# Performance work log

Measured on AMD Instinct MI355X. Metric: run time of the kernel, lower is better.

## Reference

```python
import jax, jax.numpy as jnp
import numpy as np

EPS_NORM = 1e-6
EPS_Q = 1e-5


def rmsnorm(x, g):
    var = jnp.mean(jnp.square(x), axis=-1, keepdims=True)
    return x * jax.lax.rsqrt(var + EPS_NORM) * g


def act_quant(x):
    # per-token int8 absmax fake-quant (BitNet)
    scale = 127.0 / jnp.clip(jnp.max(jnp.abs(x), axis=-1, keepdims=True), EPS_Q, None)
    return jnp.clip(jnp.round(x * scale), -128.0, 127.0) / scale


def weight_quant(w):
    # per-tensor ternary (b1.58) fake-quant
    scale = 1.0 / jnp.clip(jnp.mean(jnp.abs(w)), EPS_Q, None)
    return jnp.clip(jnp.round(w * scale), -1.0, 1.0) / scale


def ste(x, fn):
    return x + jax.lax.stop_gradient(fn(x) - x)


def bitlinear(x, w, g):
    # RMSNorm -> act fake-quant (STE) -> ternary weight fake-quant (STE) -> matmul
    xn = rmsnorm(x, g)
    xq = ste(xn, act_quant)
    wq = ste(w, weight_quant)
    return jnp.einsum('bsd,od->bso', xq, wq)


def setup_inputs() -> dict:
    key = jax.random.key(0)
    k1, k2, k3 = jax.random.split(key, 3)
    B, S, D, I = 4, 4096, 2048, 5632
    x = jax.random.normal(k1, (B, S, D), dtype=jnp.float32)
    w_gate = jax.random.normal(k2, (2 * I, D), dtype=jnp.float32) * (D ** -0.5)
    g_gate = jnp.ones((D,), dtype=jnp.float32)
    w_down = jax.random.normal(k3, (D, I), dtype=jnp.float32) * (I ** -0.5)
    g_down = jnp.ones((I,), dtype=jnp.float32)
    return {"x": x, "w_gate": w_gate, "g_gate": g_gate,
            "w_down": w_down, "g_down": g_down}


def reference(x, w_gate, g_gate, w_down, g_down):
    y = bitlinear(x, w_gate, g_gate)            # [B, S, 2*I]
    gate, v = jnp.split(y, 2, axis=-1)          # chunk(2, -1)
    swiglu_out = gate * jax.nn.sigmoid(gate) * v  # swish(gate) * v
    z = bitlinear(swiglu_out, w_down, g_down)   # [B, S, D]
    return z
```

## Files before the change

### kernel.cpp

```cpp
#include <hip/hip_runtime.h>
#include <hip/hip_bf16.h>

typedef int v4i __attribute__((ext_vector_type(4)));

#define DEV __device__ __forceinline__

DEV void gload16(const void* g, void* l){
  __builtin_amdgcn_global_load_lds((const __attribute__((address_space(1))) unsigned int*)g,
                                   (__attribute__((address_space(3))) unsigned int*)l, 16, 0, 0);
}

DEV float block_sum256(float v, float* red){
#pragma unroll
  for (int o=32;o>0;o>>=1) v += __shfl_down(v,o);
  int w = threadIdx.x>>6;
  if ((threadIdx.x&63)==0) red[w]=v;
  __syncthreads();
  v = red[0]+red[1]+red[2]+red[3];
  __syncthreads();
  return v;
}
DEV float block_max256(float v, float* red){
#pragma unroll
  for (int o=32;o>0;o>>=1) v = fmaxf(v,__shfl_down(v,o));
  int w = threadIdx.x>>6;
  if ((threadIdx.x&63)==0) red[w]=v;
  __syncthreads();
  v = fmaxf(fmaxf(red[0],red[1]),fmaxf(red[2],red[3]));
  __syncthreads();
  return v;
}

__global__ __launch_bounds__(256) void reduce_abs_kernel(const float* __restrict__ w, long n4,
                                                         float* __restrict__ partials){
  __shared__ float red[4];
  const float4* w4 = (const float4*)w;
  float s = 0.f;
  for (long i = (long)blockIdx.x*256 + threadIdx.x; i < n4; i += (long)gridDim.x*256){
    float4 v = w4[i];
    s += fabsf(v.x)+fabsf(v.y)+fabsf(v.z)+fabsf(v.w);
  }
  s = block_sum256(s, red);
  if (threadIdx.x==0) partials[blockIdx.x]=s;
}

__global__ __launch_bounds__(256) void finalize_scales_kernel(const float* __restrict__ partials,
                                                              float* __restrict__ hdr){
  __shared__ float red[4];
  float s1=0.f, s2=0.f;
  for (int i=threadIdx.x;i<1024;i+=256){ s1+=partials[i]; s2+=partials[i+1024]; }
  s1 = block_sum256(s1, red);
  s2 = block_sum256(s2, red);
  if (threadIdx.x==0){
    float m1 = s1 / 23068672.0f;
    float sc1 = 1.0f / fmaxf(m1, 1e-5f);
    hdr[0]=sc1; hdr[1]=1.0f/sc1;
    float m2 = s2 / 11534336.0f;
    float sc2 = 1.0f / fmaxf(m2, 1e-5f);
    hdr[2]=sc2; hdr[3]=1.0f/sc2;
  }
}

__global__ __launch_bounds__(256) void quant_w_kernel(const float* __restrict__ w,
                                                      signed char* __restrict__ wq, long n4,
                                                      const float* __restrict__ hdr, int hi){
  float scale = hdr[hi];
  const float4* w4 = (const float4*)w;
  unsigned* o4 = (unsigned*)wq;
  for (long i = (long)blockIdx.x*256 + threadIdx.x; i < n4; i += (long)gridDim.x*256){
    float4 v = w4[i];
    int q0 = (int)fminf(fmaxf(rintf(v.x*scale),-1.f),1.f);
    int q1 = (int)fminf(fmaxf(rintf(v.y*scale),-1.f),1.f);
    int q2 = (int)fminf(fmaxf(rintf(v.z*scale),-1.f),1.f);
    int q3 = (int)fminf(fmaxf(rintf(v.w*scale),-1.f),1.f);
    unsigned pk = (q0&0xff) | ((q1&0xff)<<8) | ((q2&0xff)<<16) | ((q3&0xff)<<24);
    o4[i] = pk;
  }
}

__global__ __launch_bounds__(256) void rms_quant_x_kernel(const float* __restrict__ x,
                                                          const float* __restrict__ g,
                                                          signed char* __restrict__ xq,
                                                          float* __restrict__ isx){
  __shared__ float red[4];
  const int row = blockIdx.x, t = threadIdx.x;
  const float* xr = x + (size_t)row*2048 + t*8;
  float4 a = *(const float4*)xr;
  float4 b = *(const float4*)(xr+4);
  float xv[8] = {a.x,a.y,a.z,a.w,b.x,b.y,b.z,b.w};
  float ss = 0.f;
#pragma unroll
  for (int i=0;i<8;i++) ss += xv[i]*xv[i];
  ss = block_sum256(ss, red);
  float rs = rsqrtf(ss*(1.0f/2048.0f) + 1e-6f);
  const float* gr = g + t*8;
  float4 ga = *(const float4*)gr;
  float4 gb = *(const float4*)(gr+4);
  float gv[8] = {ga.x,ga.y,ga.z,ga.w,gb.x,gb.y,gb.z,gb.w};
  float xn[8]; float m = 0.f;
#pragma unroll
  for (int i=0;i<8;i++){ xn[i] = xv[i]*rs*gv[i]; m = fmaxf(m, fabsf(xn[i])); }
  m = block_max256(m, red);
  float scale = 127.0f / fmaxf(m, 1e-5f);
  unsigned long long pk = 0;
#pragma unroll
  for (int i=0;i<8;i++){
    int q = (int)fminf(fmaxf(rintf(xn[i]*scale), -128.0f), 127.0f);
    pk |= (unsigned long long)(unsigned char)(signed char)q << (8*i);
  }
  *(unsigned long long*)(xq + (size_t)row*2048 + t*8) = pk;
  if (t==0) isx[row] = 1.0f/scale;
}

__global__ __launch_bounds__(256) void rms_quant_sg_kernel(const __hip_bfloat16* __restrict__ sg,
                                                           const float* __restrict__ g,
                                                           signed char* __restrict__ xq,
                                                           float* __restrict__ isx){
  __shared__ float red[4];
  const int row = blockIdx.x, t = threadIdx.x;
  const unsigned* sr = (const unsigned*)(sg + (size_t)row*5632);
  float s[22];
  float ss = 0.f;
#pragma unroll
  for (int i=0;i<11;i++){
    unsigned u = sr[t + i*256];
    float f0 = __uint_as_float(u<<16);
    float f1 = __uint_as_float(u & 0xffff0000u);
    s[2*i]=f0; s[2*i+1]=f1;
    ss += f0*f0 + f1*f1;
  }
  ss = block_sum256(ss, red);
  float rs = rsqrtf(ss*(1.0f/5632.0f) + 1e-6f);
  const float2* g2 = (const float2*)g;
  float xn[22]; float m = 0.f;
#pragma unroll
  for (int i=0;i<11;i++){
    float2 gv = g2[t + i*256];
    xn[2*i]   = s[2*i]  *rs*gv.x;
    xn[2*i+1] = s[2*i+1]*rs*gv.y;
    m = fmaxf(m, fmaxf(fabsf(xn[2*i]), fabsf(xn[2*i+1])));
  }
  m = block_max256(m, red);
  float scale = 127.0f / fmaxf(m, 1e-5f);
  short* o2 = (short*)(xq + (size_t)row*5632);
#pragma unroll
  for (int i=0;i<11;i++){
    int q0 = (int)fminf(fmaxf(rintf(xn[2*i]  *scale), -128.0f), 127.0f);
    int q1 = (int)fminf(fmaxf(rintf(xn[2*i+1]*scale), -128.0f), 127.0f);
    o2[t + i*256] = (short)((q0 & 0xff) | ((q1 & 0xff) << 8));
  }
  if (t==0) isx[row] = 1.0f/scale;
}

__global__ __launch_bounds__(512) void gemm1_swiglu_kernel(const signed char* __restrict__ A,
                                                           const signed char* __restrict__ B,
                                                           const float* __restrict__ inv_sx,
                                                           const float* __restrict__ hdr,
                                                           __hip_bfloat16* __restrict__ out){
  constexpr int K = 2048;
  constexpr int NI = 5632;
  constexpr int NT = 32;
  __shared__ __align__(16) unsigned char smem[131072];

  const int t = threadIdx.x;
  const int lid = blockIdx.x + blockIdx.y * gridDim.x;
  const int xc = lid & 7;
  const int sx = lid >> 3;
  const int ch = sx >> 5;
  const int ii = sx & 31;
  const int bm0 = (xc*8 + (ii>>2)) * 256;
  const int bc0 = (ch*4 + (ii&3)) * 128;
  const int w = t >> 6, l = t & 63;
  const int ts = w >> 2;
  const int wv = w & 3;
  const int wr = wv * 64;
  const int lr = l & 15, lg = l >> 4;

  const float inv_sw = hdr[1];

  const signed char* aSrc[2]; int aOff[2];
#pragma unroll
  for (int i=0;i<2;i++){
    int c = t + i*512, r = c>>2, kp = c&3;
    aSrc[i] = A + (size_t)(bm0 + r)*K + ((kp ^ ((r>>1)&3))*16);
    aOff[i] = c*16;
  }
  const signed char* bSrc[2]; int bOff[2];
#pragma unroll
  for (int i=0;i<2;i++){
    int c = t + i*512, r = c>>2, kp = c&3;
    int grow = ((r>>7) ? NI : 0) + bc0 + (r&127);
    bSrc[i] = B + (size_t)grow*K + ((kp ^ ((r>>1)&3))*16);
    bOff[i] = 16384 + c*16;
  }
  int aoff[4];
#pragma unroll
  for (int i=0;i<4;i++){ int row = wr + i*16 + lr; aoff[i] = row*64 + ((lg ^ ((row>>1)&3))*16); }
  int boff[8];
#pragma unroll
  for (int j=0;j<8;j++){ int row = ts*128 + j*16 + lr; boff[j] = 16384 + row*64 + ((lg ^ ((row>>1)&3))*16); }

  v4i acc[4][8] = {};

#define STAGE1(BUF, KT) { unsigned char* _b = smem + (BUF)*32768;      \
    gload16(aSrc[0] + (KT)*64, _b + aOff[0]);                          \
    gload16(aSrc[1] + (KT)*64, _b + aOff[1]);                          \
    gload16(bSrc[0] + (KT)*64, _b + bOff[0]);                          \
    gload16(bSrc[1] + (KT)*64, _b + bOff[1]); }

#define COMP1(BUF) {                                                   \
  const signed char* _bs = (const signed char*)smem + (BUF)*32768;     \
  v4i af[4], bf[8];                                                    \
  _Pragma("unroll") for (int _i=0;_i<4;_i++) af[_i] = *(const v4i*)(_bs + aoff[_i]); \
  _Pragma("unroll") for (int _j=0;_j<8;_j++) bf[_j] = *(const v4i*)(_bs + boff[_j]); \
  __builtin_amdgcn_s_setprio(1);                                       \
  _Pragma("unroll") for (int _j=0;_j<8;_j++)                           \
    _Pragma("unroll") for (int _i=0;_i<4;_i++)                         \
      acc[_i][_j] = __builtin_amdgcn_mfma_i32_16x16x64_i8(af[_i], bf[_j], acc[_i][_j], 0, 0, 0); \
  __builtin_amdgcn_s_setprio(0);                                       \
}

  STAGE1(0,0); STAGE1(1,1); STAGE1(2,2);

  for (int kt = 0; kt < NT-2; ++kt){
    asm volatile("s_waitcnt vmcnt(8)" ::: "memory");
    __builtin_amdgcn_s_barrier();
    __builtin_amdgcn_sched_barrier(0);
    COMP1(kt&3);
    __builtin_amdgcn_sched_barrier(0);
    if (kt <= NT-4) STAGE1((kt+3)&3, kt+3);
  }
  asm volatile("s_waitcnt vmcnt(4)" ::: "memory");
  __builtin_amdgcn_s_barrier();
  __builtin_amdgcn_sched_barrier(0);
  COMP1((NT-2)&3);
  __builtin_amdgcn_sched_barrier(0);
  asm volatile("s_waitcnt vmcnt(0)" ::: "memory");
  __builtin_amdgcn_s_barrier();
  __builtin_amdgcn_sched_barrier(0);
  COMP1((NT-1)&3);
  __builtin_amdgcn_sched_barrier(0);

  float* vex = (float*)smem;
  __syncthreads();
  if (ts == 1){
#pragma unroll
    for (int i=0;i<4;i++){
#pragma unroll
      for (int r=0;r<4;r++){
        int lrow = wr + i*16 + lg*4 + r;
        float f = inv_sx[bm0 + lrow] * inv_sw;
#pragma unroll
        for (int j=0;j<8;j++)
          vex[lrow*128 + j*16 + lr] = (float)acc[i][j][r] * f;
      }
    }
  }
  __syncthreads();
  if (ts == 0){
#pragma unroll
    for (int i=0;i<4;i++){
#pragma unroll
      for (int r=0;r<4;r++){
        int lrow = wr + i*16 + lg*4 + r;
        float f = inv_sx[bm0 + lrow] * inv_sw;
#pragma unroll
        for (int j=0;j<8;j++){
          float gv = (float)acc[i][j][r] * f;
          float vv = vex[lrow*128 + j*16 + lr];
          float sw = gv / (1.0f + expf(-gv)) * vv;
          acc[i][j][r] = __float_as_int(sw);
        }
      }
    }
  }
  __syncthreads();
  __hip_bfloat16* obuf = (__hip_bfloat16*)smem;
  if (ts == 0){
#pragma unroll
    for (int i=0;i<4;i++){
#pragma unroll
      for (int r=0;r<4;r++){
        int lrow = wr + i*16 + lg*4 + r;
#pragma unroll
        for (int j=0;j<8;j++)
          obuf[lrow*128 + j*16 + lr] = __float2bfloat16(__int_as_float(acc[i][j][r]));
      }
    }
  }
  __syncthreads();
#pragma unroll
  for (int it=0; it<8; ++it){
    int idx = t + it*512;
    int row = idx >> 4, c16 = idx & 15;
    *(int4*)((char*)(out + (size_t)(bm0+row)*NI + bc0) + c16*16) =
        *(const int4*)((const char*)obuf + row*256 + c16*16);
  }
#undef STAGE1
#undef COMP1
}

__global__ __launch_bounds__(256) void gemm2_kernel(const signed char* __restrict__ A,
                                                    const signed char* __restrict__ B,
                                                    const float* __restrict__ inv_sx,
                                                    const float* __restrict__ hdr,
                                                    float* __restrict__ out){
  constexpr int K = 5632;
  constexpr int N = 2048;
  constexpr int NT = 44;
  __shared__ __align__(16) unsigned char smem[65536];

  const int t = threadIdx.x;
  const int lid = blockIdx.x + blockIdx.y * gridDim.x;
  const int xc = lid & 7;
  const int sx = lid >> 3;
  const int ch = sx >> 4, ii = sx & 15;
  const int bm0 = (xc*16 + (ch>>2)*4 + (ii>>2)) * 128;
  const int bn0 = ((ch&3)*4 + (ii&3)) * 128;
  const int w = t >> 6, l = t & 63;
  const int wr = (w >> 1) * 64, wc = (w & 1) * 64;
  const int lr = l & 15, lg = l >> 4;

  const float inv_sw = hdr[3];

  const signed char *aSrc[4], *bSrc[4]; int aOff[4], bOff[4];
#pragma unroll
  for (int i=0;i<4;i++){
    int cc = t + i*256; int r = cc>>3, k = cc&7;
    aSrc[i] = A + (size_t)(bm0 + r)*K + ((k ^ (r&7))*16);
    bSrc[i] = B + (size_t)(bn0 + r)*K + ((k ^ (r&7))*16);
    aOff[i] = cc*16;
    bOff[i] = 16384 + cc*16;
  }

  v4i acc[4][4] = {};

#define STAGE2(BUF, KT) do{ unsigned char* _bb = smem + (BUF)*32768;              \
  _Pragma("unroll") for (int _i=0;_i<4;_i++){                                     \
    gload16(aSrc[_i] + (KT)*128, _bb + aOff[_i]);                                 \
    gload16(bSrc[_i] + (KT)*128, _bb + bOff[_i]); } }while(0)

#define COMP2(BUF) do{                                                            \
  const signed char* _As = (const signed char*)smem + (BUF)*32768;                \
  const signed char* _Bs = _As + 16384;                                           \
  _Pragma("unroll") for (int kk=0;kk<2;++kk){                                     \
    v4i af[4], bf[4];                                                             \
    _Pragma("unroll") for (int i=0;i<4;i++){                                      \
      int row = wr + i*16 + lr;                                                   \
      af[i] = *(const v4i*)(_As + row*128 + (((kk*4+lg) ^ (row&7))*16));          \
    }                                                                             \
    _Pragma("unroll") for (int j=0;j<4;j++){                                      \
      int row = wc + j*16 + lr;                                                   \
      bf[j] = *(const v4i*)(_Bs + row*128 + (((kk*4+lg) ^ (row&7))*16));          \
    }                                                                             \
    __builtin_amdgcn_s_setprio(1);                                                \
    _Pragma("unroll") for (int i=0;i<4;i++)                                       \
      _Pragma("unroll") for (int j=0;j<4;j++)                                     \
        acc[i][j] = __builtin_amdgcn_mfma_i32_16x16x64_i8(af[i], bf[j], acc[i][j], 0, 0, 0); \
    __builtin_amdgcn_s_setprio(0);                                                \
  } }while(0)

  STAGE2(0, 0);
  STAGE2(1, 1);
  for (int kt = 0; kt < NT-2; kt += 2){
    asm volatile("s_waitcnt vmcnt(8)" ::: "memory");
    __builtin_amdgcn_s_barrier();
    __builtin_amdgcn_sched_barrier(0);
    COMP2(0);
    __builtin_amdgcn_sched_barrier(0);
    __builtin_amdgcn_s_barrier();
    STAGE2(0, kt+2);
    asm volatile("s_waitcnt vmcnt(8)" ::: "memory");
    __builtin_amdgcn_s_barrier();
    __builtin_amdgcn_sched_barrier(0);
    COMP2(1);
    __builtin_amdgcn_sched_barrier(0);
    __builtin_amdgcn_s_barrier();
    STAGE2(1, kt+3);
  }
  asm volatile("s_waitcnt vmcnt(8)" ::: "memory");
  __builtin_amdgcn_s_barrier();
  __builtin_amdgcn_sched_barrier(0);
  COMP2(0);
  __builtin_amdgcn_sched_barrier(0);
  __builtin_amdgcn_s_barrier();
  asm volatile("s_waitcnt vmcnt(0)" ::: "memory");
  __builtin_amdgcn_s_barrier();
  __builtin_amdgcn_sched_barrier(0);
  COMP2(1);
  __builtin_amdgcn_sched_barrier(0);

#pragma unroll
  for (int i=0;i<4;i++){
#pragma unroll
    for (int r=0;r<4;r++){
      int lrow = wr + i*16 + lg*4 + r;
      float f = inv_sx[bm0 + lrow] * inv_sw;
      size_t o = (size_t)(bm0 + lrow) * N + bn0;
#pragma unroll
      for (int j=0;j<4;j++)
        out[o + wc + j*16 + lr] = (float)acc[i][j][r] * f;
    }
  }
#undef STAGE2
#undef COMP2
}

extern "C" void kernel_launch(void* const* d_in, const int* in_sizes, int n_in,
                              void* d_out, int out_size, void* d_ws, size_t ws_size,
                              hipStream_t stream) {
  const float* x      = (const float*)d_in[0];
  const float* w_gate = (const float*)d_in[1];
  const float* g_gate = (const float*)d_in[2];
  const float* w_down = (const float*)d_in[3];
  const float* g_down = (const float*)d_in[4];
  float* out = (float*)d_out;

  char* p = (char*)d_ws;
  float* hdr      = (float*)p;
  float* partials = (float*)(p + 64);
  size_t off = 8448;
  signed char* wqg = (signed char*)(p + off); off += 23068672;
  signed char* wqd = (signed char*)(p + off); off += 11534336;
  signed char* xq1 = (signed char*)(p + off); off += 33554432;
  signed char* xq2 = (signed char*)(p + off); off += 92274688;
  float* isx1 = (float*)(p + off); off += 65536;
  float* isx2 = (float*)(p + off); off += 65536;
  __hip_bfloat16* sg = (__hip_bfloat16*)(p + off); off += 184549376;

  reduce_abs_kernel<<<1024,256,0,stream>>>(w_gate, 23068672/4, partials);
  reduce_abs_kernel<<<1024,256,0,stream>>>(w_down, 11534336/4, partials+1024);
  finalize_scales_kernel<<<1,256,0,stream>>>(partials, hdr);
  quant_w_kernel<<<2048,256,0,stream>>>(w_gate, wqg, 23068672/4, hdr, 0);
  quant_w_kernel<<<1024,256,0,stream>>>(w_down, wqd, 11534336/4, hdr, 2);
  rms_quant_x_kernel<<<16384,256,0,stream>>>(x, g_gate, xq1, isx1);
  gemm1_swiglu_kernel<<<dim3(44,64),512,0,stream>>>(xq1, wqg, isx1, hdr, sg);
  rms_quant_sg_kernel<<<16384,256,0,stream>>>(sg, g_down, xq2, isx2);
  gemm2_kernel<<<dim3(16,128),256,0,stream>>>(xq2, wqd, isx2, hdr, out);
}
```

Baseline: 871.9 us.

## Halve gemm1 shared memory with double buffering and two-pass SwiGLU epilogue

Shared memory for the gate/up GEMM kernel drops from 128KB to 64KB. The 4-stage load pipeline becomes 2-stage, with an extra barrier before each buffer is refilled, and the SwiGLU exchange of the up-projection half now runs in two row-halves so it fits in 64KB. The aim is to let two 512-thread blocks share a CU for more latency hiding. In exchange the prefetch depth is shallower, and each K step and the epilogue gain extra barriers.

Result: slower. 947.4 us (+8.7%).

```diff
diff --git a/kernel.cpp b/kernel.cpp
--- a/kernel.cpp
+++ b/kernel.cpp
@@ -160,7 +160,7 @@
   constexpr int K = 2048;
   constexpr int NI = 5632;
   constexpr int NT = 32;
-  __shared__ __align__(16) unsigned char smem[131072];
+  __shared__ __align__(16) unsigned char smem[65536];
 
   const int t = threadIdx.x;
   const int lid = blockIdx.x + blockIdx.y * gridDim.x;
@@ -174,6 +174,7 @@
   const int ts = w >> 2;
   const int wv = w & 3;
   const int wr = wv * 64;
+  const int hw = wv >> 1;
   const int lr = l & 15, lg = l >> 4;
 
   const float inv_sw = hdr[1];
@@ -220,56 +221,53 @@
   __builtin_amdgcn_s_setprio(0);                                       \
 }
 
-  STAGE1(0,0); STAGE1(1,1); STAGE1(2,2);
-
-  for (int kt = 0; kt < NT-2; ++kt){
-    asm volatile("s_waitcnt vmcnt(8)" ::: "memory");
-    __builtin_amdgcn_s_barrier();
-    __builtin_amdgcn_sched_barrier(0);
-    COMP1(kt&3);
-    __builtin_amdgcn_sched_barrier(0);
-    if (kt <= NT-4) STAGE1((kt+3)&3, kt+3);
-  }
-  asm volatile("s_waitcnt vmcnt(4)" ::: "memory");
-  __builtin_amdgcn_s_barrier();
-  __builtin_amdgcn_sched_barrier(0);
-  COMP1((NT-2)&3);
-  __builtin_amdgcn_sched_barrier(0);
-  asm volatile("s_waitcnt vmcnt(0)" ::: "memory");
-  __builtin_amdgcn_s_barrier();
-  __builtin_amdgcn_sched_barrier(0);
-  COMP1((NT-1)&3);
-  __builtin_amdgcn_sched_barrier(0);
+  STAGE1(0,0); STAGE1(1,1);
+
+  for (int kt = 0; kt < NT; ++kt){
+    if (kt < NT-1) { asm volatile("s_waitcnt vmcnt(4)" ::: "memory"); }
+    else           { asm volatile("s_waitcnt vmcnt(0)" ::: "memory"); }
+    __builtin_amdgcn_s_barrier();
+    __builtin_amdgcn_sched_barrier(0);
+    COMP1(kt&1);
+    __builtin_amdgcn_sched_barrier(0);
+    __builtin_amdgcn_s_barrier();
+    if (kt < NT-2) STAGE1(kt&1, kt+2);
+  }
 
   float* vex = (float*)smem;
-  __syncthreads();
-  if (ts == 1){
-#pragma unroll
-    for (int i=0;i<4;i++){
-#pragma unroll
-      for (int r=0;r<4;r++){
-        int lrow = wr + i*16 + lg*4 + r;
-        float f = inv_sx[bm0 + lrow] * inv_sw;
-#pragma unroll
-        for (int j=0;j<8;j++)
-          vex[lrow*128 + j*16 + lr] = (float)acc[i][j][r] * f;
+#pragma unroll
+  for (int h=0; h<2; ++h){
+    __syncthreads();
+    if (ts == 1 && hw == h){
+#pragma unroll
+      for (int i=0;i<4;i++){
+#pragma unroll
+        for (int r=0;r<4;r++){
+          int lrow = wr + i*16 + lg*4 + r;
+          int lloc = lrow - h*128;
+          float f = inv_sx[bm0 + lrow] * inv_sw;
+#pragma unroll
+          for (int j=0;j<8;j++)
+            vex[lloc*128 + j*16 + lr] = (float)acc[i][j][r] * f;
+        }
       }
     }
-  }
-  __syncthreads();
-  if (ts == 0){
-#pragma unroll
-    for (int i=0;i<4;i++){
-#pragma unroll
-      for (int r=0;r<4;r++){
-        int lrow = wr + i*16 + lg*4 + r;
-        float f = inv_sx[bm0 + lrow] * inv_sw;
-#pragma unroll
-        for (int j=0;j<8;j++){
-          float gv = (float)acc[i][j][r] * f;
-          float vv = vex[lrow*128 + j*16 + lr];
-          float sw = gv / (1.0f + expf(-gv)) * vv;
-          acc[i][j][r] = __float_as_int(sw);
+    __syncthreads();
+    if (ts == 0 && hw == h){
+#pragma unroll
+      for (int i=0;i<4;i++){
+#pragma unroll
+        for (int r=0;r<4;r++){
+          int lrow = wr + i*16 + lg*4 + r;
+          int lloc = lrow - h*128;
+          float f = inv_sx[bm0 + lrow] * inv_sw;
+#pragma unroll
+          for (int j=0;j<8;j++){
+            float gv = (float)acc[i][j][r] * f;
+            float vv = vex[lloc*128 + j*16 + lr];
+            float sw = gv / (1.0f + expf(-gv)) * vv;
+            acc[i][j][r] = __float_as_int(sw);
+          }
         }
       }
     }
```

## Split gemm1 k-step into two half-phases interleaving LDS reads, prefetch, and MFMA

Applied to the files above, without the earlier changes.

Restructures the int8 gemm1 main loop so each k-tile is processed in two halves. Each half loads part of the B fragments from LDS, issues part of the global-to-LDS prefetch (A first, then B), and runs half of the MFMAs, with extra barriers between halves. The aim is to overlap LDS reads and global-load issue with matrix work across waves, in the style of a ping-pong schedule. The cost is more barriers per k-step and different vmcnt bookkeeping, and the split may add serialization.

Result: faster. 846.0 us (-3.0%).

```diff
diff --git a/kernel.cpp b/kernel.cpp
--- a/kernel.cpp
+++ b/kernel.cpp
@@ -202,44 +202,56 @@
 
   v4i acc[4][8] = {};
 
-#define STAGE1(BUF, KT) { unsigned char* _b = smem + (BUF)*32768;      \
-    gload16(aSrc[0] + (KT)*64, _b + aOff[0]);                          \
-    gload16(aSrc[1] + (KT)*64, _b + aOff[1]);                          \
-    gload16(bSrc[0] + (KT)*64, _b + bOff[0]);                          \
+#define STA1(BUF, KT) { unsigned char* _b = smem + (BUF)*32768;      \
+    gload16(aSrc[0] + (KT)*64, _b + aOff[0]);                        \
+    gload16(aSrc[1] + (KT)*64, _b + aOff[1]); }
+#define STB1(BUF, KT) { unsigned char* _b = smem + (BUF)*32768;      \
+    gload16(bSrc[0] + (KT)*64, _b + bOff[0]);                        \
     gload16(bSrc[1] + (KT)*64, _b + bOff[1]); }
 
-#define COMP1(BUF) {                                                   \
-  const signed char* _bs = (const signed char*)smem + (BUF)*32768;     \
-  v4i af[4], bf[8];                                                    \
-  _Pragma("unroll") for (int _i=0;_i<4;_i++) af[_i] = *(const v4i*)(_bs + aoff[_i]); \
-  _Pragma("unroll") for (int _j=0;_j<8;_j++) bf[_j] = *(const v4i*)(_bs + boff[_j]); \
-  __builtin_amdgcn_s_setprio(1);                                       \
-  _Pragma("unroll") for (int _j=0;_j<8;_j++)                           \
-    _Pragma("unroll") for (int _i=0;_i<4;_i++)                         \
-      acc[_i][_j] = __builtin_amdgcn_mfma_i32_16x16x64_i8(af[_i], bf[_j], acc[_i][_j], 0, 0, 0); \
-  __builtin_amdgcn_s_setprio(0);                                       \
-}
-
-  STAGE1(0,0); STAGE1(1,1); STAGE1(2,2);
-
-  for (int kt = 0; kt < NT-2; ++kt){
-    asm volatile("s_waitcnt vmcnt(8)" ::: "memory");
-    __builtin_amdgcn_s_barrier();
-    __builtin_amdgcn_sched_barrier(0);
-    COMP1(kt&3);
-    __builtin_amdgcn_sched_barrier(0);
-    if (kt <= NT-4) STAGE1((kt+3)&3, kt+3);
-  }
-  asm volatile("s_waitcnt vmcnt(4)" ::: "memory");
+  STA1(0,0); STB1(0,0);
+  STA1(1,1); STB1(1,1);
+  STA1(2,2); STB1(2,2);
+  asm volatile("s_waitcnt vmcnt(8)" ::: "memory");
   __builtin_amdgcn_s_barrier();
-  __builtin_amdgcn_sched_barrier(0);
-  COMP1((NT-2)&3);
-  __builtin_amdgcn_sched_barrier(0);
-  asm volatile("s_waitcnt vmcnt(0)" ::: "memory");
-  __builtin_amdgcn_s_barrier();
-  __builtin_amdgcn_sched_barrier(0);
-  COMP1((NT-1)&3);
-  __builtin_amdgcn_sched_barrier(0);
+
+  for (int kt = 0; kt < NT; ++kt){
+    const signed char* bs = (const signed char*)smem + (kt&3)*32768;
+    v4i af[4], bf[8];
+#pragma unroll
+    for (int i=0;i<4;i++) af[i] = *(const v4i*)(bs + aoff[i]);
+#pragma unroll
+    for (int j=0;j<4;j++) bf[j] = *(const v4i*)(bs + boff[j]);
+    if (kt < NT-3) STA1((kt+3)&3, kt+3);
+    __builtin_amdgcn_s_barrier();
+    asm volatile("s_waitcnt lgkmcnt(0)" ::: "memory");
+    __builtin_amdgcn_sched_barrier(0);
+    __builtin_amdgcn_s_setprio(1);
+#pragma unroll
+    for (int j=0;j<4;j++)
+#pragma unroll
+      for (int i=0;i<4;i++)
+        acc[i][j] = __builtin_amdgcn_mfma_i32_16x16x64_i8(af[i], bf[j], acc[i][j], 0, 0, 0);
+    __builtin_amdgcn_s_setprio(0);
+    __builtin_amdgcn_s_barrier();
+#pragma unroll
+    for (int j=4;j<8;j++) bf[j] = *(const v4i*)(bs + boff[j]);
+    if (kt < NT-3) STB1((kt+3)&3, kt+3);
+    __builtin_amdgcn_s_barrier();
+    asm volatile("s_waitcnt lgkmcnt(0)" ::: "memory");
+    __builtin_amdgcn_sched_barrier(0);
+    __builtin_amdgcn_s_setprio(1);
+#pragma unroll
+    for (int j=4;j<8;j++)
+#pragma unroll
+      for (int i=0;i<4;i++)
+        acc[i][j] = __builtin_amdgcn_mfma_i32_16x16x64_i8(af[i], bf[j], acc[i][j], 0, 0, 0);
+    __builtin_amdgcn_s_setprio(0);
+    if (kt < NT-3)       { asm volatile("s_waitcnt vmcnt(8)" ::: "memory"); }
+    else if (kt == NT-3) { asm volatile("s_waitcnt vmcnt(4)" ::: "memory"); }
+    else if (kt == NT-2) { asm volatile("s_waitcnt vmcnt(0)" ::: "memory"); }
+    __builtin_amdgcn_s_barrier();
+  }
 
   float* vex = (float*)smem;
   __syncthreads();
@@ -296,8 +308,8 @@
     *(int4*)((char*)(out + (size_t)(bm0+row)*NI + bc0) + c16*16) =
         *(const int4*)((const char*)obuf + row*256 + c16*16);
   }
-#undef STAGE1
-#undef COMP1
+#undef STA1
+#undef STB1
 }
 
 __global__ __launch_bounds__(256) void gemm2_kernel(const signed char* __restrict__ A,
```
